# Kernel optimization log

Measured on AMD Instinct MI355X. Metric: run time of the kernel, lower is better.

## Reference

```python
import jax, jax.numpy as jnp
import numpy as np

ORDER, IN_DIM, OUT_DIM, SEQ_LEN = 4096, 8, 1, 4096


def setup_inputs() -> dict:
    key = jax.random.key(0)
    ks = jax.random.split(key, 7)
    # reset_parameter uses uniform(-0.7, 0.7); A/C/L rescaled ~1/sqrt(order) for
    # numerical stability of the 4096-step linear recurrence (same math, stable values).
    sA = 0.9 * (3.0 / ORDER) ** 0.5
    sC = 0.7 / ORDER ** 0.5
    weight_a = jax.random.uniform(ks[0], (ORDER, ORDER), minval=-sA, maxval=sA, dtype=jnp.float32)
    weight_b = jax.random.uniform(ks[1], (ORDER, IN_DIM), minval=-0.7, maxval=0.7, dtype=jnp.float32)
    weight_c = jax.random.uniform(ks[2], (OUT_DIM, ORDER), minval=-sC, maxval=sC, dtype=jnp.float32)
    weight_d = jax.random.uniform(ks[3], (OUT_DIM, IN_DIM), minval=-0.7, maxval=0.7, dtype=jnp.float32)
    weight_l = jax.random.uniform(ks[4], (ORDER, 1), minval=-sC, maxval=sC, dtype=jnp.float32)
    u = jax.random.normal(ks[5], (IN_DIM, SEQ_LEN), dtype=jnp.float32)
    y_obs = jax.random.normal(ks[6], (1, SEQ_LEN), dtype=jnp.float32)
    return {"u": u, "y_obs": y_obs, "weight_a": weight_a, "weight_b": weight_b,
            "weight_c": weight_c, "weight_d": weight_d, "weight_l": weight_l}


def reference(u, y_obs, weight_a, weight_b, weight_c, weight_d, weight_l):
    # Observer (Luenberger) state-space recursion, inp_dim > 1 branch:
    #   y_t  = C h_t + D u_t
    #   h_{t+1} = A h_t + B u_t + L * (y_obs_t - y_t)
    # output = tanh(concat(y_t)) * 3, shape [out_dim, seq_len]
    order = weight_a.shape[0]
    h0 = jnp.ones((order, 1), dtype=u.dtype)  # nn.init.constant_(hidden, 1)

    def step(h, inp):
        u_t, yobs_t = inp  # u_t: [in_dim, 1], yobs_t: scalar
        y_t = weight_c @ h + weight_d @ u_t          # [out_dim, 1]
        h_next = weight_a @ h + weight_b @ u_t + weight_l * (yobs_t - y_t)
        return h_next, y_t

    u_seq = u.T[:, :, None]          # [seq_len, in_dim, 1]
    _, ys = jax.lax.scan(step, h0, (u_seq, y_obs[0]))
    y_hat = ys[:, :, 0].T            # [out_dim, seq_len]
    return jnp.tanh(y_hat) * 3
```

## Files before the change

kernel.cpp:

```cpp
#include <hip/hip_runtime.h>
#include <math.h>


constexpr int NDIM  = 4096;
constexpr int NC    = 10;
constexpr int SLAB  = 16 * 4096;
constexpr int JT    = 56;
constexpr int VAPPS = 28;
constexpr int KC    = NDIM / 32;
constexpr int TILES = NDIM / 16;

typedef float    f32x4  __attribute__((ext_vector_type(4)));
typedef _Float16 h16x8  __attribute__((ext_vector_type(8)));
typedef _Float16 f16;

__global__ __launch_bounds__(256) void k_build_a(
        const float* __restrict__ A, const float* __restrict__ C,
        const float* __restrict__ L, h16x8* __restrict__ AhSw,
        unsigned int* __restrict__ rowmaxU) {
    __shared__ float lds[64][65];
    const int R0 = (blockIdx.x & 63) * 64;
    const int C0 = (blockIdx.x >> 6) * 64;
    const int tid = threadIdx.x;
    #pragma unroll
    for (int it = 0; it < 16; ++it) {
        const int r = it * 4 + (tid >> 6);
        const int c = tid & 63;
        lds[r][c] = A[(size_t)(R0 + r) * NDIM + C0 + c]
                  - L[R0 + r] * C[C0 + c];
    }
    __syncthreads();
    if (tid < 64) {
        float mx = 0.0f;
        #pragma unroll 8
        for (int c = 0; c < 64; ++c) mx = fmaxf(mx, fabsf(lds[tid][c]));
        atomicMax(&rowmaxU[R0 + tid], __float_as_uint(mx));
    }
    #pragma unroll
    for (int half = 0; half < 2; ++half) {
        const int o = half * 256 + tid;
        const int r = o >> 3;
        const int g = o & 7;
        union { h16x8 v; f16 h[8]; } pk;
        #pragma unroll
        for (int j = 0; j < 8; ++j) pk.h[j] = (f16)lds[r][g * 8 + j];
        const int tile = (R0 >> 4) + (r >> 4);
        const int kc   = (C0 >> 5) + (g >> 2);
        const int lane = (r & 15) | ((g & 3) << 4);
        AhSw[((size_t)tile * KC + kc) * 64 + lane] = pk.v;
    }
}

__global__ __launch_bounds__(256) void k_quant_r(
        const h16x8* __restrict__ AhSw, const unsigned int* __restrict__ rowmaxU,
        signed char* __restrict__ A8r, float* __restrict__ sAr) {
    const size_t idx = (size_t)blockIdx.x * blockDim.x + threadIdx.x;
    const int lane = (int)(idx & 63);
    const int kc   = (int)((idx >> 6) & (KC - 1));
    const int tile = (int)(idx >> 13);
    const int row  = tile * 16 + (lane & 15);
    const int col  = kc * 32 + (lane >> 4) * 8;
    const float rm  = __uint_as_float(rowmaxU[row]);
    const float inv = rm > 0.0f ? 127.0f / rm : 0.0f;
    union { h16x8 v; f16 h[8]; } uh;
    uh.v = AhSw[idx];
    union { long l; signed char c[8]; } uo;
    #pragma unroll
    for (int j = 0; j < 8; ++j) {
        int qv = (int)rintf((float)uh.h[j] * inv);
        qv = qv > 127 ? 127 : (qv < -127 ? -127 : qv);
        uo.c[j] = (signed char)qv;
    }
    *(long*)(A8r + (size_t)row * NDIM + col) = uo.l;
    if (kc == 0 && (lane >> 4) == 0) sAr[row] = rm / 127.0f;
}

__global__ __launch_bounds__(256) void k_build_w0(
        const float* __restrict__ Bm, const float* __restrict__ Dm,
        const float* __restrict__ L,
        float* __restrict__ Wf, f16* __restrict__ Wh,
        unsigned int* __restrict__ rowmaxU) {
    int k = blockIdx.x * blockDim.x + threadIdx.x;
    rowmaxU[k] = 0u;
    float Lk = L[k];
    float col[16];
    #pragma unroll
    for (int c = 0; c < 8; ++c) col[c] = Bm[k * 8 + c] - Lk * Dm[c];
    col[8] = Lk; col[9] = 1.0f;
    #pragma unroll
    for (int c = 10; c < 16; ++c) col[c] = 0.0f;
    #pragma unroll
    for (int c = 0; c < 16; ++c) {
        Wf[c * NDIM + k] = col[c];
        Wh[c * NDIM + k] = (f16)col[c];
    }
}

__global__ __launch_bounds__(256) void k_stepVR(
        const h16x8* __restrict__ AhSw,
        const signed char* __restrict__ A8r, const float* __restrict__ sAr,
        const f16* __restrict__ WhIn,
        float* __restrict__ WfOut, f16* __restrict__ WhOut,
        const float* __restrict__ Cvec,
        const float* __restrict__ RpartIn, float* __restrict__ RpartOut,
        float* __restrict__ gfSlot, const int r) {
    const int tid = threadIdx.x;

    if (blockIdx.x < 128) {
        __shared__ f32x4 red[4][64];
        const int lane = tid & 63, wave = tid >> 6;
        const int mr   = lane & 15, q = lane >> 4;
        const int tp   = blockIdx.x;
        const int tile = tp * 2 + (wave >> 1);
        const int kh   = wave & 1;
        const int k0   = kh * 2048;
        const bool liveB = (mr < NC);
        const h16x8* a8 = AhSw + ((size_t)tile * KC + (size_t)kh * 64) * 64 + lane;
        const h16x8* b8 = (const h16x8*)WhIn + (((size_t)mr * NDIM + k0) >> 3) + q;

        f32x4 acc0 = {0,0,0,0}, acc1 = {0,0,0,0};
        for (int it = 0; it < 8; ++it) {
            h16x8 ra[8], rb[8];
            #pragma unroll
            for (int s = 0; s < 8; ++s) rb[s] = (h16x8){0,0,0,0,0,0,0,0};
            #pragma unroll
            for (int s = 0; s < 8; ++s) {
                const int c = it * 8 + s;
                ra[s] = a8[(size_t)c * 64];
            }
            if (liveB) {
                #pragma unroll
                for (int s = 0; s < 8; ++s) {
                    const int c = it * 8 + s;
                    rb[s] = b8[c * 4];
                }
            }
            #pragma unroll
            for (int s = 0; s < 8; ++s) {
                if (s & 1) acc1 = __builtin_amdgcn_mfma_f32_16x16x32_f16(ra[s], rb[s], acc1, 0, 0, 0);
                else       acc0 = __builtin_amdgcn_mfma_f32_16x16x32_f16(ra[s], rb[s], acc0, 0, 0, 0);
            }
        }
        red[wave][lane] = acc0 + acc1;
        __syncthreads();
        if (tid < 128) {
            const int half = tid >> 6;
            const int l    = tid & 63;
            f32x4 v = red[half * 2][l] + red[half * 2 + 1][l];
            const int col = l & 15;
            if (col < NC) {
                const int row0 = (tp * 2 + half) * 16;
                const int rb0  = row0 + ((l >> 4) << 2);
                #pragma unroll
                for (int i = 0; i < 4; ++i) {
                    WfOut[col * NDIM + rb0 + i] = v[i];
                    WhOut[col * NDIM + rb0 + i] = (f16)v[i];
                }
            }
        }
    } else {
        __shared__ float rp[4096];
        __shared__ float g8[8][33];
        __shared__ float gs[32];
        const int t = blockIdx.x - 128;

        if (r == 0) {
            if (tid < 32) gs[tid] = Cvec[t * 32 + tid];
        } else {
            #pragma unroll
            for (int i = 0; i < 16; ++i) {
                const int idx = tid + i * 256;
                rp[idx] = RpartIn[(size_t)(idx >> 5) * NDIM + t * 32 + (idx & 31)];
            }
            __syncthreads();
            {
                const int c = tid & 31, g = tid >> 5;
                float s = 0.0f;
                #pragma unroll
                for (int j = 0; j < 16; ++j) s += rp[(g * 16 + j) * 32 + c];
                g8[g][c] = s;
            }
            __syncthreads();
            if (tid < 32) {
                float s = 0.0f;
                #pragma unroll
                for (int g = 0; g < 8; ++g) s += g8[g][tid];
                gs[tid] = s;
            }
        }
        __syncthreads();
        if (tid < 32) gfSlot[t * 32 + tid] = gs[tid];

        if (r < VAPPS - 1) {
            float gl[32];
            #pragma unroll
            for (int j = 0; j < 32; ++j) gl[j] = gs[j] * sAr[t * 32 + j];
            const int c0 = tid * 16;
            float acc[16] = {};
            const int4* arow = (const int4*)(A8r + (size_t)(t * 32) * NDIM + c0);
            for (int rr = 0; rr < 32; ++rr) {
                const int4 v = arow[(size_t)rr * (NDIM / 16)];
                const float gm = gl[rr];
                const int w0 = v.x, w1 = v.y, w2 = v.z, w3 = v.w;
                #pragma unroll
                for (int b = 0; b < 4; ++b) {
                    acc[b]      += gm * (float)((w0 << (24 - 8 * b)) >> 24);
                    acc[4 + b]  += gm * (float)((w1 << (24 - 8 * b)) >> 24);
                    acc[8 + b]  += gm * (float)((w2 << (24 - 8 * b)) >> 24);
                    acc[12 + b] += gm * (float)((w3 << (24 - 8 * b)) >> 24);
                }
            }
            float4* op = (float4*)(RpartOut + (size_t)t * NDIM + c0);
            op[0] = make_float4(acc[0],  acc[1],  acc[2],  acc[3]);
            op[1] = make_float4(acc[4],  acc[5],  acc[6],  acc[7]);
            op[2] = make_float4(acc[8],  acc[9],  acc[10], acc[11]);
            op[3] = make_float4(acc[12], acc[13], acc[14], acc[15]);
        }
    }
}

__global__ __launch_bounds__(256) void k_fbatch(
        const float* __restrict__ Wall, const float* __restrict__ C,
        const float* __restrict__ gf, float* __restrict__ F) {
    const int m = blockIdx.x;
    const float* W;
    const float* vec;
    if (m <= VAPPS) { W = Wall + (size_t)m * SLAB;     vec = C; }
    else            { W = Wall + (size_t)VAPPS * SLAB; vec = gf + (size_t)(m - VAPPS) * NDIM; }
    const int tid = threadIdx.x, lane = tid & 63, wave = tid >> 6;
    float acc[NC] = {};
    for (int k = tid; k < NDIM; k += 256) {
        float ck = vec[k];
        #pragma unroll
        for (int c = 0; c < NC; ++c) acc[c] += ck * W[c * NDIM + k];
    }
    __shared__ float red[4][NC];
    #pragma unroll
    for (int c = 0; c < NC; ++c) {
        float s = acc[c];
        #pragma unroll
        for (int off = 32; off > 0; off >>= 1) s += __shfl_down(s, off);
        if (lane == 0) red[wave][c] = s;
    }
    __syncthreads();
    if (tid < NC) F[m * NC + tid] = red[0][tid] + red[1][tid] + red[2][tid] + red[3][tid];
}

__global__ __launch_bounds__(256) void k_conv(
        const float* __restrict__ F, const float* __restrict__ u,
        const float* __restrict__ yobs, const float* __restrict__ Dm,
        float* __restrict__ out) {
    __shared__ float Fl[JT * NC];
    __shared__ float zw[(JT + 256) * 9];
    const int tid = threadIdx.x;
    const int t0  = blockIdx.x * 256;
    for (int idx = tid; idx < JT * NC; idx += 256) Fl[idx] = F[idx];
    for (int idx = tid; idx < (JT + 256) * 9; idx += 256) {
        int k = idx / 9, c = idx - k * 9;
        int s = t0 - JT + k;
        float v = 0.0f;
        if (s >= 0 && s < NDIM) v = (c < 8) ? u[c * NDIM + s] : yobs[s];
        zw[idx] = v;
    }
    __syncthreads();
    const int t = t0 + tid;
    float y = (t < JT) ? Fl[t * NC + 9] : 0.0f;
    #pragma unroll
    for (int c = 0; c < 8; ++c) y += Dm[c] * u[c * NDIM + t];
    for (int j = 0; j < JT; ++j) {
        const float* fj = Fl + j * NC;
        const float* zz = zw + (tid + JT - 1 - j) * 9;
        float p = 0.0f;
        #pragma unroll
        for (int c = 0; c < 9; ++c) p += fj[c] * zz[c];
        y += p;
    }
    out[t] = 3.0f * tanhf(y);
}

extern "C" void kernel_launch(void* const* d_in, const int* in_sizes, int n_in,
                              void* d_out, int out_size, void* d_ws, size_t ws_size,
                              hipStream_t stream) {
    const float* u    = (const float*)d_in[0];
    const float* yobs = (const float*)d_in[1];
    const float* A    = (const float*)d_in[2];
    const float* Bm   = (const float*)d_in[3];
    const float* C    = (const float*)d_in[4];
    const float* Dm   = (const float*)d_in[5];
    const float* L    = (const float*)d_in[6];
    float* out = (float*)d_out;

    char* ws = (char*)d_ws;
    h16x8*        AhSw    = (h16x8*)ws;
    signed char*  A8r     = (signed char*)(ws + 33554432ull);
    float*        Wf      = (float*)(ws + 50331648ull);
    f16*          Wh      = (f16*)(ws + 57933824ull);
    float*        gf      = (float*)(ws + 61734912ull);
    float*        Rpart   = (float*)(ws + 62193664ull);
    float*        F       = (float*)(ws + 66387968ull);
    float*        sAr     = (float*)(ws + 66390208ull);
    unsigned int* rowmaxU = (unsigned int*)(ws + 66406592ull);

    constexpr size_t RPN = (size_t)128 * NDIM;

    k_build_w0<<<dim3(16), dim3(256), 0, stream>>>(Bm, Dm, L, Wf, Wh, rowmaxU);
    k_build_a<<<dim3(64 * 64), dim3(256), 0, stream>>>(A, C, L, AhSw, rowmaxU);
    k_quant_r<<<dim3(TILES * KC * 64 / 256), dim3(256), 0, stream>>>(AhSw, rowmaxU, A8r, sAr);

    for (int r = 0; r < VAPPS; ++r) {
        const size_t in   = (size_t)r * SLAB;
        const size_t out_ = (size_t)(r + 1) * SLAB;
        const float* rin  = Rpart + ((r + 1) & 1) * RPN;
        float*       rout = Rpart + (r & 1) * RPN;
        k_stepVR<<<dim3(256), dim3(256), 0, stream>>>(
            AhSw, A8r, sAr, Wh + in, Wf + out_, Wh + out_,
            C, rin, rout, gf + (size_t)r * NDIM, r);
    }

    k_fbatch<<<dim3(JT), dim3(256), 0, stream>>>(Wf, C, gf, F);
    k_conv<<<dim3(16), dim3(256), 0, stream>>>(F, u, yobs, Dm, out);
}
```

Measured before the change: 438.8 us.

## Fuse int8 quantization into A build with per-block scales, fp16 partials

Removes the separate quantization kernel and global row-max atomics by quantizing A to int8 inside the build kernel using per-64-column-block row scales. The step kernel applies these finer scales through a shared-memory table. The fp32 W copies are dropped and fbatch reads the fp16 W instead. The reduction partials are stored as fp16, which halves that traffic at the cost of precision in the partial sums and in the F coefficients.

```diff
diff --git a/kernel.cpp b/kernel.cpp
--- a/kernel.cpp
+++ b/kernel.cpp
@@ -17,8 +17,9 @@
 __global__ __launch_bounds__(256) void k_build_a(
         const float* __restrict__ A, const float* __restrict__ C,
         const float* __restrict__ L, h16x8* __restrict__ AhSw,
-        unsigned int* __restrict__ rowmaxU) {
+        signed char* __restrict__ A8r, float* __restrict__ sAg) {
     __shared__ float lds[64][65];
+    __shared__ float smax[64];
     const int R0 = (blockIdx.x & 63) * 64;
     const int C0 = (blockIdx.x >> 6) * 64;
     const int tid = threadIdx.x;
@@ -34,7 +35,22 @@
         float mx = 0.0f;
         #pragma unroll 8
         for (int c = 0; c < 64; ++c) mx = fmaxf(mx, fabsf(lds[tid][c]));
-        atomicMax(&rowmaxU[R0 + tid], __float_as_uint(mx));
+        smax[tid] = mx;
+        sAg[(size_t)(R0 + tid) * 64 + (C0 >> 6)] = mx / 127.0f;
+    }
+    __syncthreads();
+    {
+        const int r = tid >> 2, seg = tid & 3;
+        const float mx = smax[r];
+        const float inv = mx > 0.0f ? 127.0f / mx : 0.0f;
+        union { int4 v; signed char c[16]; } uo;
+        #pragma unroll
+        for (int j = 0; j < 16; ++j) {
+            int qv = (int)rintf(lds[r][seg * 16 + j] * inv);
+            qv = qv > 127 ? 127 : (qv < -127 ? -127 : qv);
+            uo.c[j] = (signed char)qv;
+        }
+        *(int4*)(A8r + (size_t)(R0 + r) * NDIM + C0 + seg * 16) = uo.v;
     }
     #pragma unroll
     for (int half = 0; half < 2; ++half) {
@@ -51,37 +67,10 @@
     }
 }
 
-__global__ __launch_bounds__(256) void k_quant_r(
-        const h16x8* __restrict__ AhSw, const unsigned int* __restrict__ rowmaxU,
-        signed char* __restrict__ A8r, float* __restrict__ sAr) {
-    const size_t idx = (size_t)blockIdx.x * blockDim.x + threadIdx.x;
-    const int lane = (int)(idx & 63);
-    const int kc   = (int)((idx >> 6) & (KC - 1));
-    const int tile = (int)(idx >> 13);
-    const int row  = tile * 16 + (lane & 15);
-    const int col  = kc * 32 + (lane >> 4) * 8;
-    const float rm  = __uint_as_float(rowmaxU[row]);
-    const float inv = rm > 0.0f ? 127.0f / rm : 0.0f;
-    union { h16x8 v; f16 h[8]; } uh;
-    uh.v = AhSw[idx];
-    union { long l; signed char c[8]; } uo;
-    #pragma unroll
-    for (int j = 0; j < 8; ++j) {
-        int qv = (int)rintf((float)uh.h[j] * inv);
-        qv = qv > 127 ? 127 : (qv < -127 ? -127 : qv);
-        uo.c[j] = (signed char)qv;
-    }
-    *(long*)(A8r + (size_t)row * NDIM + col) = uo.l;
-    if (kc == 0 && (lane >> 4) == 0) sAr[row] = rm / 127.0f;
-}
-
 __global__ __launch_bounds__(256) void k_build_w0(
         const float* __restrict__ Bm, const float* __restrict__ Dm,
-        const float* __restrict__ L,
-        float* __restrict__ Wf, f16* __restrict__ Wh,
-        unsigned int* __restrict__ rowmaxU) {
+        const float* __restrict__ L, f16* __restrict__ Wh) {
     int k = blockIdx.x * blockDim.x + threadIdx.x;
-    rowmaxU[k] = 0u;
     float Lk = L[k];
     float col[16];
     #pragma unroll
@@ -90,19 +79,15 @@
     #pragma unroll
     for (int c = 10; c < 16; ++c) col[c] = 0.0f;
     #pragma unroll
-    for (int c = 0; c < 16; ++c) {
-        Wf[c * NDIM + k] = col[c];
-        Wh[c * NDIM + k] = (f16)col[c];
-    }
+    for (int c = 0; c < 16; ++c) Wh[c * NDIM + k] = (f16)col[c];
 }
 
 __global__ __launch_bounds__(256) void k_stepVR(
         const h16x8* __restrict__ AhSw,
-        const signed char* __restrict__ A8r, const float* __restrict__ sAr,
-        const f16* __restrict__ WhIn,
-        float* __restrict__ WfOut, f16* __restrict__ WhOut,
+        const signed char* __restrict__ A8r, const float* __restrict__ sAg,
+        const f16* __restrict__ WhIn, f16* __restrict__ WhOut,
         const float* __restrict__ Cvec,
-        const float* __restrict__ RpartIn, float* __restrict__ RpartOut,
+        const f16* __restrict__ RpartIn, f16* __restrict__ RpartOut,
         float* __restrict__ gfSlot, const int r) {
     const int tid = threadIdx.x;
 
@@ -152,32 +137,34 @@
                 const int row0 = (tp * 2 + half) * 16;
                 const int rb0  = row0 + ((l >> 4) << 2);
                 #pragma unroll
-                for (int i = 0; i < 4; ++i) {
-                    WfOut[col * NDIM + rb0 + i] = v[i];
+                for (int i = 0; i < 4; ++i)
                     WhOut[col * NDIM + rb0 + i] = (f16)v[i];
-                }
             }
         }
     } else {
-        __shared__ float rp[4096];
+        __shared__ f16   rp[128][32];
         __shared__ float g8[8][33];
         __shared__ float gs[32];
+        __shared__ float gsc[32][64];
         const int t = blockIdx.x - 128;
 
         if (r == 0) {
             if (tid < 32) gs[tid] = Cvec[t * 32 + tid];
         } else {
-            #pragma unroll
-            for (int i = 0; i < 16; ++i) {
-                const int idx = tid + i * 256;
-                rp[idx] = RpartIn[(size_t)(idx >> 5) * NDIM + t * 32 + (idx & 31)];
+            {
+                const int p = tid >> 1, half = tid & 1;
+                const h16x8* src = (const h16x8*)(RpartIn
+                        + (size_t)p * NDIM + t * 32 + half * 16);
+                h16x8 v0 = src[0], v1 = src[1];
+                *(h16x8*)&rp[p][half * 16]     = v0;
+                *(h16x8*)&rp[p][half * 16 + 8] = v1;
             }
             __syncthreads();
             {
                 const int c = tid & 31, g = tid >> 5;
                 float s = 0.0f;
                 #pragma unroll
-                for (int j = 0; j < 16; ++j) s += rp[(g * 16 + j) * 32 + c];
+                for (int j = 0; j < 16; ++j) s += (float)rp[g * 16 + j][c];
                 g8[g][c] = s;
             }
             __syncthreads();
@@ -192,15 +179,20 @@
         if (tid < 32) gfSlot[t * 32 + tid] = gs[tid];
 
         if (r < VAPPS - 1) {
-            float gl[32];
-            #pragma unroll
-            for (int j = 0; j < 32; ++j) gl[j] = gs[j] * sAr[t * 32 + j];
+            #pragma unroll
+            for (int i = 0; i < 8; ++i) {
+                const int idx = tid + i * 256;
+                const int rr = idx >> 6, g = idx & 63;
+                gsc[rr][g] = gs[rr] * sAg[(size_t)(t * 32 + rr) * 64 + g];
+            }
+            __syncthreads();
             const int c0 = tid * 16;
+            const int g0 = tid >> 2;
             float acc[16] = {};
             const int4* arow = (const int4*)(A8r + (size_t)(t * 32) * NDIM + c0);
             for (int rr = 0; rr < 32; ++rr) {
                 const int4 v = arow[(size_t)rr * (NDIM / 16)];
-                const float gm = gl[rr];
+                const float gm = gsc[rr][g0];
                 const int w0 = v.x, w1 = v.y, w2 = v.z, w3 = v.w;
                 #pragma unroll
                 for (int b = 0; b < 4; ++b) {
@@ -210,29 +202,33 @@
                     acc[12 + b] += gm * (float)((w3 << (24 - 8 * b)) >> 24);
                 }
             }
-            float4* op = (float4*)(RpartOut + (size_t)t * NDIM + c0);
-            op[0] = make_float4(acc[0],  acc[1],  acc[2],  acc[3]);
-            op[1] = make_float4(acc[4],  acc[5],  acc[6],  acc[7]);
-            op[2] = make_float4(acc[8],  acc[9],  acc[10], acc[11]);
-            op[3] = make_float4(acc[12], acc[13], acc[14], acc[15]);
+            union { h16x8 h; int4 i4; } o0, o1;
+            #pragma unroll
+            for (int j = 0; j < 8; ++j) {
+                o0.h[j] = (f16)acc[j];
+                o1.h[j] = (f16)acc[8 + j];
+            }
+            h16x8* op = (h16x8*)(RpartOut + (size_t)t * NDIM + c0);
+            op[0] = o0.h;
+            op[1] = o1.h;
         }
     }
 }
 
 __global__ __launch_bounds__(256) void k_fbatch(
-        const float* __restrict__ Wall, const float* __restrict__ C,
+        const f16* __restrict__ Wh, const float* __restrict__ C,
         const float* __restrict__ gf, float* __restrict__ F) {
     const int m = blockIdx.x;
-    const float* W;
+    const f16* W;
     const float* vec;
-    if (m <= VAPPS) { W = Wall + (size_t)m * SLAB;     vec = C; }
-    else            { W = Wall + (size_t)VAPPS * SLAB; vec = gf + (size_t)(m - VAPPS) * NDIM; }
+    if (m <= VAPPS) { W = Wh + (size_t)m * SLAB;     vec = C; }
+    else            { W = Wh + (size_t)VAPPS * SLAB; vec = gf + (size_t)(m - VAPPS) * NDIM; }
     const int tid = threadIdx.x, lane = tid & 63, wave = tid >> 6;
     float acc[NC] = {};
     for (int k = tid; k < NDIM; k += 256) {
         float ck = vec[k];
         #pragma unroll
-        for (int c = 0; c < NC; ++c) acc[c] += ck * W[c * NDIM + k];
+        for (int c = 0; c < NC; ++c) acc[c] += ck * (float)W[c * NDIM + k];
     }
     __shared__ float red[4][NC];
     #pragma unroll
@@ -291,32 +287,29 @@
     float* out = (float*)d_out;
 
     char* ws = (char*)d_ws;
-    h16x8*        AhSw    = (h16x8*)ws;
-    signed char*  A8r     = (signed char*)(ws + 33554432ull);
-    float*        Wf      = (float*)(ws + 50331648ull);
-    f16*          Wh      = (f16*)(ws + 57933824ull);
-    float*        gf      = (float*)(ws + 61734912ull);
-    float*        Rpart   = (float*)(ws + 62193664ull);
-    float*        F       = (float*)(ws + 66387968ull);
-    float*        sAr     = (float*)(ws + 66390208ull);
-    unsigned int* rowmaxU = (unsigned int*)(ws + 66406592ull);
+    h16x8*       AhSw  = (h16x8*)ws;
+    signed char* A8r   = (signed char*)(ws + 33554432ull);
+    float*       sAg   = (float*)(ws + 50331648ull);
+    f16*         Wh    = (f16*)(ws + 51380224ull);
+    float*       gf    = (float*)(ws + 55181312ull);
+    f16*         RpartH= (f16*)(ws + 55640064ull);
+    float*       F     = (float*)(ws + 57737216ull);
 
     constexpr size_t RPN = (size_t)128 * NDIM;
 
-    k_build_w0<<<dim3(16), dim3(256), 0, stream>>>(Bm, Dm, L, Wf, Wh, rowmaxU);
-    k_build_a<<<dim3(64 * 64), dim3(256), 0, stream>>>(A, C, L, AhSw, rowmaxU);
-    k_quant_r<<<dim3(TILES * KC * 64 / 256), dim3(256), 0, stream>>>(AhSw, rowmaxU, A8r, sAr);
+    k_build_w0<<<dim3(16), dim3(256), 0, stream>>>(Bm, Dm, L, Wh);
+    k_build_a<<<dim3(64 * 64), dim3(256), 0, stream>>>(A, C, L, AhSw, A8r, sAg);
 
     for (int r = 0; r < VAPPS; ++r) {
         const size_t in   = (size_t)r * SLAB;
         const size_t out_ = (size_t)(r + 1) * SLAB;
-        const float* rin  = Rpart + ((r + 1) & 1) * RPN;
-        float*       rout = Rpart + (r & 1) * RPN;
+        const f16* rin  = RpartH + ((r + 1) & 1) * RPN;
+        f16*       rout = RpartH + (r & 1) * RPN;
         k_stepVR<<<dim3(256), dim3(256), 0, stream>>>(
-            AhSw, A8r, sAr, Wh + in, Wf + out_, Wh + out_,
+            AhSw, A8r, sAg, Wh + in, Wh + out_,
             C, rin, rout, gf + (size_t)r * NDIM, r);
     }
 
-    k_fbatch<<<dim3(JT), dim3(256), 0, stream>>>(Wf, C, gf, F);
+    k_fbatch<<<dim3(JT), dim3(256), 0, stream>>>(Wh, C, gf, F);
     k_conv<<<dim3(16), dim3(256), 0, stream>>>(F, u, yobs, Dm, out);
 }
```

Measured after the change: 425.9 us. -3.0%, faster.
